# Performance work log

Hardware: AMD Instinct MI355X
Metric: run time of the kernel (lower is better)

## Reference

```python
import jax, jax.numpy as jnp
import numpy as np

R, N, B = 3, 8192, 4096
IN_DIM, HID, OUT = 256, 128, 64
EPS = 1e-5


def _bn(x, g, b):
    # BatchNorm1d in training mode: biased batch stats over dim 0
    m = jnp.mean(x, axis=0)
    v = jnp.var(x, axis=0)
    return (x - m) * jax.lax.rsqrt(v + EPS) * g + b


def setup_inputs() -> dict:
    key = jax.random.key(0)
    k1, k2, k3, k4, k5 = jax.random.split(key, 5)
    features = jax.random.normal(k1, (N, IN_DIM), dtype=jnp.float32)
    u = jax.random.uniform(k2, (R, N, N), dtype=jnp.float32)
    adj = (u < 0.01).astype(jnp.float32)
    batch_nodes = jax.random.randint(k3, (B,), 0, N, dtype=jnp.int32)
    w1 = jax.random.uniform(k4, (IN_DIM, HID), dtype=jnp.float32)  # torch.rand init
    w2 = jax.random.uniform(k5, (HID, OUT), dtype=jnp.float32)
    return {
        "features": features, "adj": adj, "batch_nodes": batch_nodes,
        "w1": w1, "w2": w2,
        "gamma1": jnp.ones((IN_DIM,), jnp.float32), "beta1": jnp.zeros((IN_DIM,), jnp.float32),
        "gamma2": jnp.ones((OUT,), jnp.float32), "beta2": jnp.zeros((OUT,), jnp.float32),
    }


def reference(features, adj, batch_nodes, w1, w2, gamma1, beta1, gamma2, beta2):
    # gather batch subgraph
    x = features[batch_nodes]                       # [B, IN_DIM]
    bA = jnp.take(jnp.take(adj, batch_nodes, axis=1), batch_nodes, axis=2)  # [R, B, B]
    xn = _bn(x, gamma1, beta1)                      # shared across relations

    def per_relation(badj):
        A = badj + jnp.eye(B, dtype=badj.dtype)
        # D_mx.inverse().sqrt() of a diagonal degree matrix == diag(deg^-1/2)
        dinv = jax.lax.rsqrt(jnp.sum(A, axis=1))    # [B]
        A_hat = A * dinv[:, None] * dinv[None, :]   # D^-1/2 A D^-1/2
        h1 = jax.nn.sigmoid(jax.nn.elu((A_hat @ xn) @ w1))   # conv1 + sigmoid
        h2 = jax.nn.elu((A_hat @ h1) @ w2)                   # conv2
        return _bn(h2, gamma2, beta2)

    embed = jax.vmap(per_relation)(bA)              # [R, B, OUT]
    return jax.nn.relu(jnp.mean(embed, axis=0))     # [B, OUT]
```

## Files before the change

### kernel.cpp

```cpp
#include <hip/hip_runtime.h>
#include <hip/hip_bf16.h>

#define RR 3
#define NN 8192
#define BB 4096
#define IN_DIM 256
#define HID 128
#define OUT 64
#define CAPD 128
#define EPS 1e-5f
#define MWN (NN / 64)

__global__ __launch_bounds__(256) void k1_bn1_prep_k(const float* __restrict__ feat,
                                                     const int* __restrict__ bn,
                                                     const float* __restrict__ g1,
                                                     const float* __restrict__ b1,
                                                     float* __restrict__ af,
                                                     float* __restrict__ bfv,
                                                     unsigned long long* __restrict__ memb,
                                                     unsigned short* __restrict__ rankg,
                                                     unsigned short* __restrict__ nodeof,
                                                     float* __restrict__ multf,
                                                     int* __restrict__ Ucnt,
                                                     unsigned short* __restrict__ pos2slot) {
    __shared__ int smult[NN];
    __shared__ unsigned short srank[NN];
    __shared__ unsigned long long smemb[MWN];
    __shared__ int sbase[MWN + 1];
    __shared__ float ps[4], pq[4];
    int t = threadIdx.x;
    if (blockIdx.x < IN_DIM) {
        int c = blockIdx.x;
        float s = 0.f, q = 0.f;
        for (int i = t; i < BB; i += 256) {
            float v = feat[(size_t)bn[i] * IN_DIM + c];
            s += v; q += v * v;
        }
        int lane = t & 63, wv = t >> 6;
        for (int o = 32; o; o >>= 1) { s += __shfl_down(s, o); q += __shfl_down(q, o); }
        if (lane == 0) { ps[wv] = s; pq[wv] = q; }
        __syncthreads();
        if (t == 0) {
            float S = ps[0] + ps[1] + ps[2] + ps[3];
            float Q = pq[0] + pq[1] + pq[2] + pq[3];
            float m = S / BB;
            float rs = rsqrtf(Q / BB - m * m + EPS);
            float a = rs * g1[c];
            af[c]  = a;
            bfv[c] = b1[c] - m * a;
        }
        return;
    }
    for (int u = t; u < NN; u += 256) smult[u] = 0;
    __syncthreads();
    for (int i = t; i < BB; i += 256) atomicAdd(&smult[bn[i]], 1);
    __syncthreads();
    if (t < MWN) {
        unsigned long long w = 0;
        for (int b = 0; b < 64; ++b) if (smult[t * 64 + b]) w |= (1ull << b);
        smemb[t] = w;
        memb[t] = w;
    }
    __syncthreads();
    if (t == 0) {
        int acc = 0;
        for (int m = 0; m < MWN; ++m) { sbase[m] = acc; acc += (int)__popcll(smemb[m]); }
        sbase[MWN] = acc;
        *Ucnt = acc;
    }
    __syncthreads();
    if (t < MWN) {
        unsigned long long w = smemb[t];
        int p = sbase[t];
        while (w) {
            int b = __builtin_ctzll(w); w &= w - 1;
            int u = t * 64 + b;
            srank[u] = (unsigned short)p;
            rankg[u] = (unsigned short)p;
            nodeof[p] = (unsigned short)u;
            multf[p]  = (float)smult[u];
            ++p;
        }
    }
    __syncthreads();
    for (int i = t; i < BB; i += 256) pos2slot[i] = srank[bn[i]];
}

__global__ __launch_bounds__(256) void build_k(const float* __restrict__ adj,
                                               const unsigned short* __restrict__ nodeof,
                                               const int* __restrict__ Ucnt,
                                               const unsigned long long* __restrict__ memb,
                                               const unsigned short* __restrict__ rankg,
                                               const float* __restrict__ multf,
                                               unsigned* __restrict__ cols,
                                               int* __restrict__ cnt,
                                               float* __restrict__ dinv) {
    int blk = blockIdx.x;
    int r = blk >> 12, s = blk & (BB - 1);
    if (s >= *Ucnt) return;
    int u = nodeof[s];
    __shared__ unsigned char nib[2048];
    __shared__ unsigned int rawb[256];
    __shared__ unsigned long long sel[MWN];
    __shared__ int sbase[MWN + 1];
    __shared__ float pdeg[4];
    int t = threadIdx.x;
    const float4* ar4 = (const float4*)(adj + ((size_t)r * NN + u) * NN);
    #pragma unroll
    for (int ch = 0; ch < 8; ++ch) {
        float4 v = ar4[ch * 256 + t];
        nib[ch * 256 + t] = (unsigned char)((v.x != 0.f) | ((v.y != 0.f) << 1) |
                                            ((v.z != 0.f) << 2) | ((v.w != 0.f) << 3));
    }
    __syncthreads();
    {
        unsigned long long x = *(const unsigned long long*)&nib[t * 8];
        x = (x | (x >> 4))  & 0x00FF00FF00FF00FFull;
        x = (x | (x >> 8))  & 0x0000FFFF0000FFFFull;
        x = (x | (x >> 16));
        rawb[t] = (unsigned int)x;
    }
    __syncthreads();
    if (t < MWN) {
        unsigned long long w = ((unsigned long long)rawb[2 * t + 1] << 32) | rawb[2 * t];
        sel[t] = w & memb[t];
    }
    __syncthreads();
    if (t < 64) {
        int p0 = (int)__popcll(sel[2 * t]);
        int p1 = (int)__popcll(sel[2 * t + 1]);
        int x = p0 + p1, xs = x;
        for (int o = 1; o < 64; o <<= 1) { int y = __shfl_up(xs, o); if (t >= o) xs += y; }
        sbase[2 * t]     = xs - x;
        sbase[2 * t + 1] = xs - p1;
        if (t == 63) sbase[MWN] = xs;
    }
    __syncthreads();
    float wdeg = 0.f;
    if (t < MWN) {
        unsigned long long w = sel[t];
        int p = sbase[t];
        unsigned* cb = cols + (size_t)blk * CAPD;
        while (w) {
            int b = __builtin_ctzll(w); w &= w - 1;
            int v = t * 64 + b;
            int rv = rankg[v];
            if (p < CAPD) cb[p] = ((unsigned)rv << 13) | (unsigned)v;
            wdeg += multf[rv];
            ++p;
        }
    }
    int lane = t & 63, wv = t >> 6;
    for (int o = 32; o; o >>= 1) wdeg += __shfl_down(wdeg, o);
    if (lane == 0) pdeg[wv] = wdeg;
    __syncthreads();
    if (t == 0) {
        int tot = sbase[MWN];
        cnt[blk] = tot < CAPD ? tot : CAPD;
        dinv[blk] = rsqrtf(pdeg[0] + pdeg[1] + pdeg[2] + pdeg[3] + 1.0f);
    }
}

__global__ __launch_bounds__(256) void aggmlp1_k(const float* __restrict__ feat,
                                                 const unsigned* __restrict__ cols,
                                                 const int* __restrict__ cnt,
                                                 const float* __restrict__ dinv,
                                                 const float* __restrict__ multf,
                                                 const unsigned short* __restrict__ nodeof,
                                                 const int* __restrict__ Ucnt,
                                                 const float* __restrict__ af,
                                                 const float* __restrict__ bfv,
                                                 const float* __restrict__ w1,
                                                 float* __restrict__ h1) {
    int blk = blockIdx.x;
    int r = blk >> 8, base = (blk & 255) << 4;
    int U = *Ucnt;
    if (base >= U) return;
    int t = threadIdx.x, lane = t & 63, wv = t >> 6;
    __shared__ unsigned short snode[16][CAPD];
    __shared__ float swl[16][CAPD];
    __shared__ float ys[16][IN_DIM];
    __shared__ float sdii[16], ssw[16];
    __shared__ int sn[16];
    for (int s16 = wv; s16 < 16; s16 += 4) {
        int slot = base + s16;
        int n = (slot < U) ? cnt[(r << 12) + slot] : 0;
        if (lane == 0) { sn[s16] = n; sdii[s16] = (slot < U) ? dinv[(r << 12) + slot] : 0.f; }
        size_t cb = ((size_t)(r << 12) + slot) * CAPD;
        float swsum = 0.f;
        for (int idx = lane; idx < n; idx += 64) {
            unsigned e = cols[cb + idx];
            int sl = e >> 13;
            snode[s16][idx] = (unsigned short)(e & 8191u);
            float w = multf[sl] * dinv[(r << 12) + sl];
            swl[s16][idx] = w;
            swsum += w;
        }
        for (int o = 32; o; o >>= 1) swsum += __shfl_down(swsum, o);
        if (lane == 0) ssw[s16] = swsum;
    }
    __syncthreads();
    int c4 = lane << 2;
    for (int j = 0; j < 4; ++j) {
        int s16 = (wv << 2) + j;
        int slot = base + s16;
        if (slot >= U) { *(float4*)&ys[s16][c4] = make_float4(0.f, 0.f, 0.f, 0.f); continue; }
        int n = sn[s16];
        float di = sdii[s16];
        float4 v = ((const float4*)(feat + (size_t)nodeof[slot] * IN_DIM))[lane];
        float4 acc;
        acc.x = di * v.x; acc.y = di * v.y; acc.z = di * v.z; acc.w = di * v.w;
        #pragma unroll 4
        for (int k = 0; k < n; ++k) {
            float w = swl[s16][k];
            float4 x = ((const float4*)(feat + (size_t)snode[s16][k] * IN_DIM))[lane];
            acc.x += w * x.x; acc.y += w * x.y; acc.z += w * x.z; acc.w += w * x.w;
        }
        float f = di * (di + ssw[s16]);
        float4 a4 = *(const float4*)(af + c4);
        float4 b4 = *(const float4*)(bfv + c4);
        float4 o;
        o.x = a4.x * (acc.x * di) + b4.x * f;
        o.y = a4.y * (acc.y * di) + b4.y * f;
        o.z = a4.z * (acc.z * di) + b4.z * f;
        o.w = a4.w * (acc.w * di) + b4.w * f;
        *(float4*)&ys[s16][c4] = o;
    }
    __syncthreads();
    int c = t & 127, g = t >> 7;
    float acc[8] = {0.f};
    for (int k = 0; k < IN_DIM; ++k) {
        float wvl = w1[k * HID + c];
        #pragma unroll
        for (int j = 0; j < 8; ++j) acc[j] += ys[g * 8 + j][k] * wvl;
    }
    #pragma unroll
    for (int j = 0; j < 8; ++j) {
        int slot = base + g * 8 + j;
        if (slot < U) {
            float z = acc[j];
            float e = z > 0.f ? z : expm1f(z);
            h1[((size_t)(r << 12) + slot) * HID + c] = 1.f / (1.f + expf(-e));
        }
    }
}

__global__ __launch_bounds__(256) void aggmlp2_k(const float* __restrict__ h1,
                                                 const unsigned* __restrict__ cols,
                                                 const int* __restrict__ cnt,
                                                 const float* __restrict__ dinv,
                                                 const float* __restrict__ multf,
                                                 const int* __restrict__ Ucnt,
                                                 const float* __restrict__ w2,
                                                 float* __restrict__ h2) {
    int blk = blockIdx.x;
    int r = blk >> 8, base = (blk & 255) << 4;
    int U = *Ucnt;
    if (base >= U) return;
    int t = threadIdx.x, lane = t & 63, wv = t >> 6;
    __shared__ unsigned short scl[16][CAPD];
    __shared__ float swl[16][CAPD];
    __shared__ float ys[16][HID];
    __shared__ float sdii[16];
    __shared__ int sn[16];
    for (int s16 = wv; s16 < 16; s16 += 4) {
        int slot = base + s16;
        int n = (slot < U) ? cnt[(r << 12) + slot] : 0;
        if (lane == 0) { sn[s16] = n; sdii[s16] = (slot < U) ? dinv[(r << 12) + slot] : 0.f; }
        size_t cb = ((size_t)(r << 12) + slot) * CAPD;
        for (int idx = lane; idx < n; idx += 64) {
            unsigned e = cols[cb + idx];
            int sl = e >> 13;
            scl[s16][idx] = (unsigned short)sl;
            swl[s16][idx] = multf[sl] * dinv[(r << 12) + sl];
        }
    }
    __syncthreads();
    const float* h1r = h1 + ((size_t)(r << 12)) * HID;
    int c2 = lane << 1;
    for (int j = 0; j < 4; ++j) {
        int s16 = (wv << 2) + j;
        int slot = base + s16;
        if (slot >= U) { ys[s16][c2] = 0.f; ys[s16][c2 + 1] = 0.f; continue; }
        int n = sn[s16];
        float di = sdii[s16];
        float2 v = ((const float2*)(h1r + (size_t)slot * HID))[lane];
        float ax = di * v.x, ay = di * v.y;
        #pragma unroll 4
        for (int k = 0; k < n; ++k) {
            float w = swl[s16][k];
            float2 x = ((const float2*)(h1r + (size_t)scl[s16][k] * HID))[lane];
            ax += w * x.x; ay += w * x.y;
        }
        ys[s16][c2] = ax * di;
        ys[s16][c2 + 1] = ay * di;
    }
    __syncthreads();
    int c = t & 63, g = t >> 6;
    float acc[4] = {0.f};
    for (int k = 0; k < HID; ++k) {
        float wvl = w2[k * OUT + c];
        #pragma unroll
        for (int j = 0; j < 4; ++j) acc[j] += ys[g * 4 + j][k] * wvl;
    }
    #pragma unroll
    for (int j = 0; j < 4; ++j) {
        int slot = base + g * 4 + j;
        if (slot < U) {
            float z = acc[j];
            h2[((size_t)(r << 12) + slot) * OUT + c] = z > 0.f ? z : expm1f(z);
        }
    }
}

__global__ __launch_bounds__(256) void bn2_stats_k(const float* __restrict__ h2,
                                                   const float* __restrict__ multf,
                                                   const int* __restrict__ Ucnt,
                                                   float* __restrict__ m2,
                                                   float* __restrict__ rs2) {
    int ro = blockIdx.x;
    int r = ro >> 6, o = ro & (OUT - 1);
    int U = *Ucnt;
    float s = 0.f, q = 0.f;
    for (int sl = threadIdx.x; sl < U; sl += 256) {
        float m = multf[sl];
        float v = h2[(size_t)((r << 12) + sl) * OUT + o];
        s += m * v; q += m * v * v;
    }
    int lane = threadIdx.x & 63, wv = threadIdx.x >> 6;
    for (int off = 32; off; off >>= 1) { s += __shfl_down(s, off); q += __shfl_down(q, off); }
    __shared__ float ps[4], pq[4];
    if (lane == 0) { ps[wv] = s; pq[wv] = q; }
    __syncthreads();
    if (threadIdx.x == 0) {
        float S = ps[0] + ps[1] + ps[2] + ps[3];
        float Q = pq[0] + pq[1] + pq[2] + pq[3];
        float m = S / BB;
        float v = Q / BB - m * m;
        m2[ro] = m;
        rs2[ro] = rsqrtf(v + EPS);
    }
}

__global__ __launch_bounds__(256) void finalize_k(const float* __restrict__ h2,
                                                  const unsigned short* __restrict__ pos2slot,
                                                  const float* __restrict__ m2,
                                                  const float* __restrict__ rs2,
                                                  const float* __restrict__ g2,
                                                  const float* __restrict__ b2,
                                                  float* __restrict__ out) {
    int idx = blockIdx.x * 256 + threadIdx.x;
    if (idx >= BB * OUT) return;
    int i = idx >> 6, o = idx & (OUT - 1);
    int sl = pos2slot[i];
    float s = 0.f;
    for (int r = 0; r < RR; ++r) {
        float v = h2[(size_t)((r << 12) + sl) * OUT + o];
        s += (v - m2[r * OUT + o]) * rs2[r * OUT + o] * g2[o] + b2[o];
    }
    s *= (1.0f / RR);
    out[idx] = s > 0.f ? s : 0.f;
}

extern "C" void kernel_launch(void* const* d_in, const int* in_sizes, int n_in,
                              void* d_out, int out_size, void* d_ws, size_t ws_size,
                              hipStream_t stream) {
    const float* feat = (const float*)d_in[0];
    const float* adj  = (const float*)d_in[1];
    const int*   bn   = (const int*)d_in[2];
    const float* w1   = (const float*)d_in[3];
    const float* w2   = (const float*)d_in[4];
    const float* g1   = (const float*)d_in[5];
    const float* b1   = (const float*)d_in[6];
    const float* g2   = (const float*)d_in[7];
    const float* b2   = (const float*)d_in[8];
    float* out = (float*)d_out;

    char* ws = (char*)d_ws;
    size_t off = 0;
    auto alloc = [&](size_t bytes) { size_t o = off; off += (bytes + 255) & ~(size_t)255; return o; };
    unsigned long long* memb = (unsigned long long*)(ws + alloc(MWN * 8));
    unsigned short* rankg    = (unsigned short*)(ws + alloc(NN * 2));
    unsigned short* nodeof   = (unsigned short*)(ws + alloc(BB * 2));
    float* multf             = (float*)(ws + alloc(BB * 4));
    int* Ucnt                = (int*)(ws + alloc(4));
    unsigned short* pos2slot = (unsigned short*)(ws + alloc(BB * 2));
    float* af                = (float*)(ws + alloc(IN_DIM * 4));
    float* bfv               = (float*)(ws + alloc(IN_DIM * 4));
    float* m2                = (float*)(ws + alloc(RR * OUT * 4));
    float* rs2               = (float*)(ws + alloc(RR * OUT * 4));
    unsigned* cols           = (unsigned*)(ws + alloc((size_t)RR * BB * CAPD * 4));
    int* cnt                 = (int*)(ws + alloc((size_t)RR * BB * 4));
    float* dinv              = (float*)(ws + alloc((size_t)RR * BB * 4));
    float* h1                = (float*)(ws + alloc((size_t)RR * BB * HID * 4));
    float* h2                = (float*)(ws + alloc((size_t)RR * BB * OUT * 4));

    k1_bn1_prep_k<<<IN_DIM + 1, 256, 0, stream>>>(feat, bn, g1, b1, af, bfv,
                                                  memb, rankg, nodeof, multf, Ucnt, pos2slot);
    build_k<<<RR * BB, 256, 0, stream>>>(adj, nodeof, Ucnt, memb, rankg, multf, cols, cnt, dinv);
    aggmlp1_k<<<RR * (BB / 16), 256, 0, stream>>>(feat, cols, cnt, dinv, multf, nodeof, Ucnt,
                                                  af, bfv, w1, h1);
    aggmlp2_k<<<RR * (BB / 16), 256, 0, stream>>>(h1, cols, cnt, dinv, multf, Ucnt, w2, h2);
    bn2_stats_k<<<RR * OUT, 256, 0, stream>>>(h2, multf, Ucnt, m2, rs2);
    finalize_k<<<(BB * OUT + 255) / 256, 256, 0, stream>>>(h2, pos2slot, m2, rs2, g2, b2, out);
}
```

Before: 154.1 us.

## Fuse BN2 statistics into conv2 epilogue via atomics and vectorize dense matmul loops

Drops the separate bn2_stats kernel. aggmlp2 now accumulates multiplicity-weighted sum and sum-of-squares per relation and channel in shared memory and adds them to global buffers with atomics. The buffers are zeroed in the prep kernel, and finalize computes mean and rsqrt from them. The dense W1/W2 matmul loops also read ys as float4 and four weights per step. This saves a kernel launch and a re-read of h2, at the cost of atomic contention and non-deterministic float summation order.

```diff
diff --git a/kernel.cpp b/kernel.cpp
--- a/kernel.cpp
+++ b/kernel.cpp
@@ -22,7 +22,9 @@
                                                      unsigned short* __restrict__ nodeof,
                                                      float* __restrict__ multf,
                                                      int* __restrict__ Ucnt,
-                                                     unsigned short* __restrict__ pos2slot) {
+                                                     unsigned short* __restrict__ pos2slot,
+                                                     float* __restrict__ Sb,
+                                                     float* __restrict__ Qb) {
     __shared__ int smult[NN];
     __shared__ unsigned short srank[NN];
     __shared__ unsigned long long smemb[MWN];
@@ -51,6 +53,7 @@
         }
         return;
     }
+    if (t < RR * OUT) { Sb[t] = 0.f; Qb[t] = 0.f; }
     for (int u = t; u < NN; u += 256) smult[u] = 0;
     __syncthreads();
     for (int i = t; i < BB; i += 256) atomicAdd(&smult[bn[i]], 1);
@@ -229,10 +232,16 @@
     __syncthreads();
     int c = t & 127, g = t >> 7;
     float acc[8] = {0.f};
-    for (int k = 0; k < IN_DIM; ++k) {
-        float wvl = w1[k * HID + c];
+    for (int k = 0; k < IN_DIM; k += 4) {
+        float wa = w1[(size_t)(k + 0) * HID + c];
+        float wb = w1[(size_t)(k + 1) * HID + c];
+        float wc = w1[(size_t)(k + 2) * HID + c];
+        float wd = w1[(size_t)(k + 3) * HID + c];
         #pragma unroll
-        for (int j = 0; j < 8; ++j) acc[j] += ys[g * 8 + j][k] * wvl;
+        for (int j = 0; j < 8; ++j) {
+            float4 y4 = *(const float4*)&ys[g * 8 + j][k];
+            acc[j] += y4.x * wa + y4.y * wb + y4.z * wc + y4.w * wd;
+        }
     }
     #pragma unroll
     for (int j = 0; j < 8; ++j) {
@@ -252,7 +261,9 @@
                                                  const float* __restrict__ multf,
                                                  const int* __restrict__ Ucnt,
                                                  const float* __restrict__ w2,
-                                                 float* __restrict__ h2) {
+                                                 float* __restrict__ h2,
+                                                 float* __restrict__ Sb,
+                                                 float* __restrict__ Qb) {
     int blk = blockIdx.x;
     int r = blk >> 8, base = (blk & 255) << 4;
     int U = *Ucnt;
@@ -263,6 +274,7 @@
     __shared__ float ys[16][HID];
     __shared__ float sdii[16];
     __shared__ int sn[16];
+    __shared__ float rS[4][OUT], rQ[4][OUT];
     for (int s16 = wv; s16 < 16; s16 += 4) {
         int slot = base + s16;
         int n = (slot < U) ? cnt[(r << 12) + slot] : 0;
@@ -298,54 +310,44 @@
     __syncthreads();
     int c = t & 63, g = t >> 6;
     float acc[4] = {0.f};
-    for (int k = 0; k < HID; ++k) {
-        float wvl = w2[k * OUT + c];
+    for (int k = 0; k < HID; k += 4) {
+        float wa = w2[(size_t)(k + 0) * OUT + c];
+        float wb = w2[(size_t)(k + 1) * OUT + c];
+        float wc = w2[(size_t)(k + 2) * OUT + c];
+        float wd = w2[(size_t)(k + 3) * OUT + c];
         #pragma unroll
-        for (int j = 0; j < 4; ++j) acc[j] += ys[g * 4 + j][k] * wvl;
-    }
+        for (int j = 0; j < 4; ++j) {
+            float4 y4 = *(const float4*)&ys[g * 4 + j][k];
+            acc[j] += y4.x * wa + y4.y * wb + y4.z * wc + y4.w * wd;
+        }
+    }
+    float pS = 0.f, pQ = 0.f;
     #pragma unroll
     for (int j = 0; j < 4; ++j) {
         int slot = base + g * 4 + j;
         if (slot < U) {
             float z = acc[j];
-            h2[((size_t)(r << 12) + slot) * OUT + c] = z > 0.f ? z : expm1f(z);
-        }
-    }
-}
-
-__global__ __launch_bounds__(256) void bn2_stats_k(const float* __restrict__ h2,
-                                                   const float* __restrict__ multf,
-                                                   const int* __restrict__ Ucnt,
-                                                   float* __restrict__ m2,
-                                                   float* __restrict__ rs2) {
-    int ro = blockIdx.x;
-    int r = ro >> 6, o = ro & (OUT - 1);
-    int U = *Ucnt;
-    float s = 0.f, q = 0.f;
-    for (int sl = threadIdx.x; sl < U; sl += 256) {
-        float m = multf[sl];
-        float v = h2[(size_t)((r << 12) + sl) * OUT + o];
-        s += m * v; q += m * v * v;
-    }
-    int lane = threadIdx.x & 63, wv = threadIdx.x >> 6;
-    for (int off = 32; off; off >>= 1) { s += __shfl_down(s, off); q += __shfl_down(q, off); }
-    __shared__ float ps[4], pq[4];
-    if (lane == 0) { ps[wv] = s; pq[wv] = q; }
-    __syncthreads();
-    if (threadIdx.x == 0) {
-        float S = ps[0] + ps[1] + ps[2] + ps[3];
-        float Q = pq[0] + pq[1] + pq[2] + pq[3];
-        float m = S / BB;
-        float v = Q / BB - m * m;
-        m2[ro] = m;
-        rs2[ro] = rsqrtf(v + EPS);
+            float e = z > 0.f ? z : expm1f(z);
+            h2[((size_t)(r << 12) + slot) * OUT + c] = e;
+            float m = multf[slot];
+            pS += m * e;
+            pQ += m * e * e;
+        }
+    }
+    rS[g][c] = pS; rQ[g][c] = pQ;
+    __syncthreads();
+    if (g == 0) {
+        float S = rS[0][c] + rS[1][c] + rS[2][c] + rS[3][c];
+        float Q = rQ[0][c] + rQ[1][c] + rQ[2][c] + rQ[3][c];
+        atomicAdd(&Sb[r * OUT + c], S);
+        atomicAdd(&Qb[r * OUT + c], Q);
     }
 }
 
 __global__ __launch_bounds__(256) void finalize_k(const float* __restrict__ h2,
                                                   const unsigned short* __restrict__ pos2slot,
-                                                  const float* __restrict__ m2,
-                                                  const float* __restrict__ rs2,
+                                                  const float* __restrict__ Sb,
+                                                  const float* __restrict__ Qb,
                                                   const float* __restrict__ g2,
                                                   const float* __restrict__ b2,
                                                   float* __restrict__ out) {
@@ -355,8 +357,11 @@
     int sl = pos2slot[i];
     float s = 0.f;
     for (int r = 0; r < RR; ++r) {
+        float S = Sb[r * OUT + o], Q = Qb[r * OUT + o];
+        float m = S / BB;
+        float rs = rsqrtf(Q / BB - m * m + EPS);
         float v = h2[(size_t)((r << 12) + sl) * OUT + o];
-        s += (v - m2[r * OUT + o]) * rs2[r * OUT + o] * g2[o] + b2[o];
+        s += (v - m) * rs * g2[o] + b2[o];
     }
     s *= (1.0f / RR);
     out[idx] = s > 0.f ? s : 0.f;
@@ -387,8 +392,8 @@
     unsigned short* pos2slot = (unsigned short*)(ws + alloc(BB * 2));
     float* af                = (float*)(ws + alloc(IN_DIM * 4));
     float* bfv               = (float*)(ws + alloc(IN_DIM * 4));
-    float* m2                = (float*)(ws + alloc(RR * OUT * 4));
-    float* rs2               = (float*)(ws + alloc(RR * OUT * 4));
+    float* Sb                = (float*)(ws + alloc(RR * OUT * 4));
+    float* Qb                = (float*)(ws + alloc(RR * OUT * 4));
     unsigned* cols           = (unsigned*)(ws + alloc((size_t)RR * BB * CAPD * 4));
     int* cnt                 = (int*)(ws + alloc((size_t)RR * BB * 4));
     float* dinv              = (float*)(ws + alloc((size_t)RR * BB * 4));
@@ -396,11 +401,12 @@
     float* h2                = (float*)(ws + alloc((size_t)RR * BB * OUT * 4));
 
     k1_bn1_prep_k<<<IN_DIM + 1, 256, 0, stream>>>(feat, bn, g1, b1, af, bfv,
-                                                  memb, rankg, nodeof, multf, Ucnt, pos2slot);
+                                                  memb, rankg, nodeof, multf, Ucnt, pos2slot,
+                                                  Sb, Qb);
     build_k<<<RR * BB, 256, 0, stream>>>(adj, nodeof, Ucnt, memb, rankg, multf, cols, cnt, dinv);
     aggmlp1_k<<<RR * (BB / 16), 256, 0, stream>>>(feat, cols, cnt, dinv, multf, nodeof, Ucnt,
                                                   af, bfv, w1, h1);
-    aggmlp2_k<<<RR * (BB / 16), 256, 0, stream>>>(h1, cols, cnt, dinv, multf, Ucnt, w2, h2);
-    bn2_stats_k<<<RR * OUT, 256, 0, stream>>>(h2, multf, Ucnt, m2, rs2);
-    finalize_k<<<(BB * OUT + 255) / 256, 256, 0, stream>>>(h2, pos2slot, m2, rs2, g2, b2, out);
-}
+    aggmlp2_k<<<RR * (BB / 16), 256, 0, stream>>>(h1, cols, cnt, dinv, multf, Ucnt, w2, h2,
+                                                  Sb, Qb);
+    finalize_k<<<(BB * OUT + 255) / 256, 256, 0, stream>>>(h2, pos2slot, Sb, Qb, g2, b2, out);
+}
```

After: 191.9 us. +24.5%, slower.

## Reorder GCN matmuls to project before aggregation, sharing X·W1 across relations

Applied to the files above, without the earlier changes.

Uses associativity (A·X)·W = A·(X·W) to project the batch-normalized features through W1 once, shared by all three relations, before sparse aggregation. The first aggregation now gathers 128-wide rows instead of 256-wide ones, and the second layer likewise projects through W2 before aggregating 64-wide rows. The BN shift term is folded into a precomputed bias vector c1. This halves gather traffic and removes the per-relation 256x128 matmul, at the cost of an extra kernel launch and an extra intermediate buffer.

```diff
diff --git a/kernel.cpp b/kernel.cpp
--- a/kernel.cpp
+++ b/kernel.cpp
@@ -161,25 +161,63 @@
     }
 }
 
-__global__ __launch_bounds__(256) void aggmlp1_k(const float* __restrict__ feat,
-                                                 const unsigned* __restrict__ cols,
-                                                 const int* __restrict__ cnt,
-                                                 const float* __restrict__ dinv,
-                                                 const float* __restrict__ multf,
-                                                 const unsigned short* __restrict__ nodeof,
-                                                 const int* __restrict__ Ucnt,
-                                                 const float* __restrict__ af,
-                                                 const float* __restrict__ bfv,
-                                                 const float* __restrict__ w1,
-                                                 float* __restrict__ h1) {
+__global__ __launch_bounds__(256) void z1_k(const float* __restrict__ feat,
+                                            const unsigned short* __restrict__ nodeof,
+                                            const int* __restrict__ Ucnt,
+                                            const float* __restrict__ af,
+                                            const float* __restrict__ bfv,
+                                            const float* __restrict__ w1,
+                                            float* __restrict__ z1,
+                                            float* __restrict__ c1) {
+    int base = blockIdx.x << 4;
+    int U = *Ucnt;
+    int t = threadIdx.x;
+    if (base < U) {
+        __shared__ float ys[16][IN_DIM];
+        float a = af[t];
+        #pragma unroll
+        for (int s = 0; s < 16; ++s) {
+            int slot = base + s;
+            ys[s][t] = (slot < U) ? feat[(size_t)nodeof[slot] * IN_DIM + t] * a : 0.f;
+        }
+        __syncthreads();
+        int c = t & 127, g = t >> 7;
+        float acc[8] = {0.f};
+        for (int k = 0; k < IN_DIM; ++k) {
+            float wvl = w1[k * HID + c];
+            #pragma unroll
+            for (int j = 0; j < 8; ++j) acc[j] += ys[g * 8 + j][k] * wvl;
+        }
+        #pragma unroll
+        for (int j = 0; j < 8; ++j) {
+            int slot = base + g * 8 + j;
+            if (slot < U) z1[(size_t)slot * HID + c] = acc[j];
+        }
+    }
+    if (blockIdx.x == 0 && t < HID) {
+        float cc = 0.f;
+        for (int k = 0; k < IN_DIM; ++k) cc += bfv[k] * w1[k * HID + t];
+        c1[t] = cc;
+    }
+}
+
+__global__ __launch_bounds__(256) void agg1z_k(const float* __restrict__ z1,
+                                               const unsigned* __restrict__ cols,
+                                               const int* __restrict__ cnt,
+                                               const float* __restrict__ dinv,
+                                               const float* __restrict__ multf,
+                                               const int* __restrict__ Ucnt,
+                                               const float* __restrict__ c1,
+                                               const float* __restrict__ w2,
+                                               float* __restrict__ z2) {
     int blk = blockIdx.x;
     int r = blk >> 8, base = (blk & 255) << 4;
     int U = *Ucnt;
     if (base >= U) return;
     int t = threadIdx.x, lane = t & 63, wv = t >> 6;
-    __shared__ unsigned short snode[16][CAPD];
+    __shared__ unsigned short scl[16][CAPD];
     __shared__ float swl[16][CAPD];
-    __shared__ float ys[16][IN_DIM];
+    __shared__ float ys[16][HID];
     __shared__ float sdii[16], ssw[16];
     __shared__ int sn[16];
     for (int s16 = wv; s16 < 16; s16 += 4) {
@@ -191,7 +229,7 @@
         for (int idx = lane; idx < n; idx += 64) {
             unsigned e = cols[cb + idx];
             int sl = e >> 13;
-            snode[s16][idx] = (unsigned short)(e & 8191u);
+            scl[s16][idx] = (unsigned short)sl;
             float w = multf[sl] * dinv[(r << 12) + sl];
             swl[s16][idx] = w;
             swsum += w;
@@ -200,58 +238,50 @@
         if (lane == 0) ssw[s16] = swsum;
     }
     __syncthreads();
-    int c4 = lane << 2;
+    int c2 = lane << 1;
     for (int j = 0; j < 4; ++j) {
         int s16 = (wv << 2) + j;
         int slot = base + s16;
-        if (slot >= U) { *(float4*)&ys[s16][c4] = make_float4(0.f, 0.f, 0.f, 0.f); continue; }
+        if (slot >= U) { ys[s16][c2] = 0.f; ys[s16][c2 + 1] = 0.f; continue; }
         int n = sn[s16];
         float di = sdii[s16];
-        float4 v = ((const float4*)(feat + (size_t)nodeof[slot] * IN_DIM))[lane];
-        float4 acc;
-        acc.x = di * v.x; acc.y = di * v.y; acc.z = di * v.z; acc.w = di * v.w;
+        float2 v = ((const float2*)(z1 + (size_t)slot * HID))[lane];
+        float ax = di * v.x, ay = di * v.y;
         #pragma unroll 4
         for (int k = 0; k < n; ++k) {
             float w = swl[s16][k];
-            float4 x = ((const float4*)(feat + (size_t)snode[s16][k] * IN_DIM))[lane];
-            acc.x += w * x.x; acc.y += w * x.y; acc.z += w * x.z; acc.w += w * x.w;
+            float2 x = ((const float2*)(z1 + (size_t)scl[s16][k] * HID))[lane];
+            ax += w * x.x; ay += w * x.y;
         }
         float f = di * (di + ssw[s16]);
-        float4 a4 = *(const float4*)(af + c4);
-        float4 b4 = *(const float4*)(bfv + c4);
-        float4 o;
-        o.x = a4.x * (acc.x * di) + b4.x * f;
-        o.y = a4.y * (acc.y * di) + b4.y * f;
-        o.z = a4.z * (acc.z * di) + b4.z * f;
-        o.w = a4.w * (acc.w * di) + b4.w * f;
-        *(float4*)&ys[s16][c4] = o;
-    }
-    __syncthreads();
-    int c = t & 127, g = t >> 7;
-    float acc[8] = {0.f};
-    for (int k = 0; k < IN_DIM; ++k) {
-        float wvl = w1[k * HID + c];
+        float zx = ax * di + f * c1[c2];
+        float zy = ay * di + f * c1[c2 + 1];
+        float ex = zx > 0.f ? zx : expm1f(zx);
+        float ey = zy > 0.f ? zy : expm1f(zy);
+        ys[s16][c2]     = 1.f / (1.f + expf(-ex));
+        ys[s16][c2 + 1] = 1.f / (1.f + expf(-ey));
+    }
+    __syncthreads();
+    int c = t & 63, g = t >> 6;
+    float acc[4] = {0.f};
+    for (int k = 0; k < HID; ++k) {
+        float wvl = w2[k * OUT + c];
         #pragma unroll
-        for (int j = 0; j < 8; ++j) acc[j] += ys[g * 8 + j][k] * wvl;
+        for (int j = 0; j < 4; ++j) acc[j] += ys[g * 4 + j][k] * wvl;
     }
     #pragma unroll
-    for (int j = 0; j < 8; ++j) {
-        int slot = base + g * 8 + j;
-        if (slot < U) {
-            float z = acc[j];
-            float e = z > 0.f ? z : expm1f(z);
-            h1[((size_t)(r << 12) + slot) * HID + c] = 1.f / (1.f + expf(-e));
-        }
-    }
-}
-
-__global__ __launch_bounds__(256) void aggmlp2_k(const float* __restrict__ h1,
+    for (int j = 0; j < 4; ++j) {
+        int slot = base + g * 4 + j;
+        if (slot < U) z2[((size_t)(r << 12) + slot) * OUT + c] = acc[j];
+    }
+}
+
+__global__ __launch_bounds__(256) void agg2act_k(const float* __restrict__ z2,
                                                  const unsigned* __restrict__ cols,
                                                  const int* __restrict__ cnt,
                                                  const float* __restrict__ dinv,
                                                  const float* __restrict__ multf,
                                                  const int* __restrict__ Ucnt,
-                                                 const float* __restrict__ w2,
                                                  float* __restrict__ h2) {
     int blk = blockIdx.x;
     int r = blk >> 8, base = (blk & 255) << 4;
@@ -260,7 +290,6 @@
     int t = threadIdx.x, lane = t & 63, wv = t >> 6;
     __shared__ unsigned short scl[16][CAPD];
     __shared__ float swl[16][CAPD];
-    __shared__ float ys[16][HID];
     __shared__ float sdii[16];
     __shared__ int sn[16];
     for (int s16 = wv; s16 < 16; s16 += 4) {
@@ -276,40 +305,20 @@
         }
     }
     __syncthreads();
-    const float* h1r = h1 + ((size_t)(r << 12)) * HID;
-    int c2 = lane << 1;
+    const float* z2r = z2 + ((size_t)(r << 12)) * OUT;
     for (int j = 0; j < 4; ++j) {
         int s16 = (wv << 2) + j;
         int slot = base + s16;
-        if (slot >= U) { ys[s16][c2] = 0.f; ys[s16][c2 + 1] = 0.f; continue; }
+        if (slot >= U) continue;
         int n = sn[s16];
         float di = sdii[s16];
-        float2 v = ((const float2*)(h1r + (size_t)slot * HID))[lane];
-        float ax = di * v.x, ay = di * v.y;
+        float acc = di * z2r[(size_t)slot * OUT + lane];
         #pragma unroll 4
         for (int k = 0; k < n; ++k) {
-            float w = swl[s16][k];
-            float2 x = ((const float2*)(h1r + (size_t)scl[s16][k] * HID))[lane];
-            ax += w * x.x; ay += w * x.y;
-        }
-        ys[s16][c2] = ax * di;
-        ys[s16][c2 + 1] = ay * di;
-    }
-    __syncthreads();
-    int c = t & 63, g = t >> 6;
-    float acc[4] = {0.f};
-    for (int k = 0; k < HID; ++k) {
-        float wvl = w2[k * OUT + c];
-        #pragma unroll
-        for (int j = 0; j < 4; ++j) acc[j] += ys[g * 4 + j][k] * wvl;
-    }
-    #pragma unroll
-    for (int j = 0; j < 4; ++j) {
-        int slot = base + g * 4 + j;
-        if (slot < U) {
-            float z = acc[j];
-            h2[((size_t)(r << 12) + slot) * OUT + c] = z > 0.f ? z : expm1f(z);
-        }
+            acc += swl[s16][k] * z2r[(size_t)scl[s16][k] * OUT + lane];
+        }
+        float z = acc * di;
+        h2[((size_t)(r << 12) + slot) * OUT + lane] = z > 0.f ? z : expm1f(z);
     }
 }
 
@@ -387,20 +396,22 @@
     unsigned short* pos2slot = (unsigned short*)(ws + alloc(BB * 2));
     float* af                = (float*)(ws + alloc(IN_DIM * 4));
     float* bfv               = (float*)(ws + alloc(IN_DIM * 4));
+    float* c1                = (float*)(ws + alloc(HID * 4));
     float* m2                = (float*)(ws + alloc(RR * OUT * 4));
     float* rs2               = (float*)(ws + alloc(RR * OUT * 4));
     unsigned* cols           = (unsigned*)(ws + alloc((size_t)RR * BB * CAPD * 4));
     int* cnt                 = (int*)(ws + alloc((size_t)RR * BB * 4));
     float* dinv              = (float*)(ws + alloc((size_t)RR * BB * 4));
-    float* h1                = (float*)(ws + alloc((size_t)RR * BB * HID * 4));
+    float* z1                = (float*)(ws + alloc((size_t)BB * HID * 4));
+    float* z2                = (float*)(ws + alloc((size_t)RR * BB * OUT * 4));
     float* h2                = (float*)(ws + alloc((size_t)RR * BB * OUT * 4));
 
     k1_bn1_prep_k<<<IN_DIM + 1, 256, 0, stream>>>(feat, bn, g1, b1, af, bfv,
                                                   memb, rankg, nodeof, multf, Ucnt, pos2slot);
     build_k<<<RR * BB, 256, 0, stream>>>(adj, nodeof, Ucnt, memb, rankg, multf, cols, cnt, dinv);
-    aggmlp1_k<<<RR * (BB / 16), 256, 0, stream>>>(feat, cols, cnt, dinv, multf, nodeof, Ucnt,
-                                                  af, bfv, w1, h1);
-    aggmlp2_k<<<RR * (BB / 16), 256, 0, stream>>>(h1, cols, cnt, dinv, multf, Ucnt, w2, h2);
+    z1_k<<<BB / 16, 256, 0, stream>>>(feat, nodeof, Ucnt, af, bfv, w1, z1, c1);
+    agg1z_k<<<RR * (BB / 16), 256, 0, stream>>>(z1, cols, cnt, dinv, multf, Ucnt, c1, w2, z2);
+    agg2act_k<<<RR * (BB / 16), 256, 0, stream>>>(z2, cols, cnt, dinv, multf, Ucnt, h2);
     bn2_stats_k<<<RR * OUT, 256, 0, stream>>>(h2, multf, Ucnt, m2, rs2);
     finalize_k<<<(BB * OUT + 255) / 256, 256, 0, stream>>>(h2, pos2slot, m2, rs2, g2, b2, out);
 }
```

Result: slower. 158.5 us (+2.8%).
